# Kernel optimization log

Measured on AMD Instinct MI355X. Metric: run time of the kernel, lower is better.

## Reference

```python
import jax, jax.numpy as jnp
import numpy as np

N_NODES = 50000
N_EDGES = 1600000
HID = 128
NF = 128
NG = 50
NL = 6
CUTOFF = 20.0
NSEG = 64


def _ssp(x):
    # ShiftedSoftplus: softplus(x) - log(2)
    return jax.nn.softplus(x) - jnp.log(2.0).astype(x.dtype)


def setup_inputs() -> dict:
    key = jax.random.key(0)
    ks = jax.random.split(key, 24)
    s = 0.05
    inp = {
        "h": jax.random.normal(ks[0], (N_NODES, HID), dtype=jnp.float32),
        "pos": jax.random.normal(ks[1], (N_NODES, 3), dtype=jnp.float32),
        "edge_index": jax.random.randint(ks[2], (2, N_EDGES), 0, N_NODES, dtype=jnp.int64),
        "batch": jnp.sort(jax.random.randint(ks[3], (N_NODES,), 0, NSEG, dtype=jnp.int64)),
        # per-interaction-block params, stacked over NL layers (weights in [in, out] layout)
        "mlp_w1": jax.random.normal(ks[4], (NL, NG, NF), dtype=jnp.float32) * s,
        "mlp_b1": jnp.zeros((NL, NF), dtype=jnp.float32),
        "mlp_w2": jax.random.normal(ks[5], (NL, NF, NF), dtype=jnp.float32) * s,
        "mlp_b2": jnp.zeros((NL, NF), dtype=jnp.float32),
        "conv_lin1_w": jax.random.normal(ks[6], (NL, HID, NF), dtype=jnp.float32) * s,  # no bias
        "conv_lin2_w": jax.random.normal(ks[7], (NL, NF, HID), dtype=jnp.float32) * s,
        "conv_lin2_b": jnp.zeros((NL, HID), dtype=jnp.float32),
        "lin_w": jax.random.normal(ks[8], (NL, HID, HID), dtype=jnp.float32) * s,
        "lin_b": jnp.zeros((NL, HID), dtype=jnp.float32),
        # readout head
        "out1_w": jax.random.normal(ks[9], (HID, HID // 2), dtype=jnp.float32) * s,
        "out1_b": jnp.zeros((HID // 2,), dtype=jnp.float32),
        "out2_w": jax.random.normal(ks[10], (HID // 2, 1), dtype=jnp.float32) * s,
        "out2_b": jnp.zeros((1,), dtype=jnp.float32),
    }
    return inp


def reference(h, pos, edge_index, batch, mlp_w1, mlp_b1, mlp_w2, mlp_b2,
              conv_lin1_w, conv_lin2_w, conv_lin2_b, lin_w, lin_b,
              out1_w, out1_b, out2_w, out2_b):
    src = edge_index[0]  # j (messages gathered here)
    dst = edge_index[1]  # i (messages aggregated here)
    n = h.shape[0]

    # edge distances from positions (RadiusInteractionGraph.forward)
    diff = pos[src] - pos[dst]                       # [E, 3]
    d = jnp.sqrt(jnp.sum(diff * diff, axis=-1))      # [E]

    # GaussianSmearing
    offset = jnp.linspace(0.0, CUTOFF, NG, dtype=h.dtype)
    coeff = -0.5 / (offset[1] - offset[0]) ** 2
    edge_attr = jnp.exp(coeff * (d[:, None] - offset[None, :]) ** 2)  # [E, NG]

    # cosine cutoff envelope
    C = 0.5 * (jnp.cos(d * jnp.pi / CUTOFF) + 1.0)   # [E]

    for l in range(NL):
        # continuous filter from edge features
        W = _ssp(edge_attr @ mlp_w1[l] + mlp_b1[l]) @ mlp_w2[l] + mlp_b2[l]  # [E, NF]
        W = W * C[:, None]
        # CFConv: lin1 -> gather x_j -> * W -> scatter-add -> lin2
        hx = h @ conv_lin1_w[l]                       # [N, NF]
        msg = hx[src] * W                             # [E, NF]
        agg = jax.ops.segment_sum(msg, dst, num_segments=n)  # [N, NF]
        hc = agg @ conv_lin2_w[l] + conv_lin2_b[l]    # [N, HID]
        # InteractionBlock: act then lin, residual add in SchNet.forward
        h = h + (_ssp(hc) @ lin_w[l] + lin_b[l])

    # readout head
    o = _ssp(h @ out1_w + out1_b) @ out2_w + out2_b   # [N, 1]
    # 'add' readout over molecules
    return jax.ops.segment_sum(o, batch, num_segments=NSEG)  # [NSEG, 1]
```

## Files before the change

### kernel.cpp

```cpp
#include <hip/hip_runtime.h>
#include <math.h>

#define N_NODES 50000
#define N_EDGES 1600000
#define HID 128
#define NF 128
#define NG 50
#define NL 6
#define NSEG 64
#define TAB2 4096
#define CUTOFF 20.0f
#define LOG2F_ 0.6931471805599453f

typedef unsigned short u16;
typedef __attribute__((ext_vector_type(8))) short short8;
typedef __attribute__((ext_vector_type(8))) unsigned short ushort8;
typedef __attribute__((ext_vector_type(4))) float f32x4;

__device__ __forceinline__ float ssp(float x){
  float sp = fmaxf(x, 0.f) + log1pf(expf(-fabsf(x)));
  return sp - LOG2F_;
}
__device__ __forceinline__ float b2f(u16 u){
  unsigned v = ((unsigned)u) << 16; float f; __builtin_memcpy(&f, &v, 4); return f;
}
__device__ __forceinline__ u16 f2b(float f){
  unsigned u; __builtin_memcpy(&u, &f, 4);
  u += 0x7FFFu + ((u >> 16) & 1u);
  return (u16)(u >> 16);
}
__device__ __forceinline__ int swz(int row, int colb){
  return row*256 + (colb ^ ((row & 15) << 4));
}

__global__ __launch_bounds__(256) void k_dist(const int* __restrict__ ei,
                                              const float* __restrict__ pos,
                                              float* __restrict__ dist,
                                              int* __restrict__ deg){
  for (int e = blockIdx.x*blockDim.x + threadIdx.x; e < N_EDGES; e += gridDim.x*blockDim.x){
    int s = ei[e], t = ei[N_EDGES + e];
    float dx = pos[3*s]   - pos[3*t];
    float dy = pos[3*s+1] - pos[3*t+1];
    float dz = pos[3*s+2] - pos[3*t+2];
    dist[e] = sqrtf(dx*dx + dy*dy + dz*dz);
    atomicAdd(&deg[t], 1);
  }
}

__global__ __launch_bounds__(1024) void k_scan(const int* __restrict__ deg, int* __restrict__ row_start){
  __shared__ int sums[1024];
  const int t = threadIdx.x;
  const int CH = (N_NODES + 1023) / 1024;
  const int base = t * CH;
  int s = 0;
  for (int i = 0; i < CH; i++){ int idx = base + i; if (idx < N_NODES) s += deg[idx]; }
  sums[t] = s; __syncthreads();
  for (int off = 1; off < 1024; off <<= 1){
    int v = (t >= off) ? sums[t - off] : 0;
    __syncthreads();
    sums[t] += v;
    __syncthreads();
  }
  int run = (t == 0) ? 0 : sums[t - 1];
  for (int i = 0; i < CH; i++){
    int idx = base + i;
    if (idx < N_NODES){ row_start[idx] = run; run += deg[idx]; }
  }
  if (t == 1023) row_start[N_NODES] = run;
}

__global__ __launch_bounds__(256) void k_scatter(const int* __restrict__ ei,
                                                 const float* __restrict__ dist,
                                                 const int* __restrict__ row_start,
                                                 int* __restrict__ cursor,
                                                 unsigned* __restrict__ csr_pack){
  const float INV_STEP = (TAB2 - 1) / CUTOFF;
  for (int e = blockIdx.x*blockDim.x + threadIdx.x; e < N_EDGES; e += gridDim.x*blockDim.x){
    int dn = ei[N_EDGES + e];
    int slot = atomicAdd(&cursor[dn], 1);
    int p = row_start[dn] + slot;
    int j = (int)(dist[e] * INV_STEP + 0.5f);
    if (j > TAB2 - 1) j = TAB2 - 1;
    csr_pack[p] = ((unsigned)j << 16) | (unsigned)ei[e];
  }
}

__global__ __launch_bounds__(128) void k_table(const float* __restrict__ w1, const float* __restrict__ b1,
                                               const float* __restrict__ w2, const float* __restrict__ b2,
                                               u16* __restrict__ tab){
  int l = blockIdx.x / TAB2, j = blockIdx.x % TAB2;
  int tid = threadIdx.x;
  float d = j * (CUTOFF / (TAB2 - 1));
  __shared__ float ea[NG];
  __shared__ float sbuf[NF];
  if (tid < NG){
    const float gstep = CUTOFF / (NG - 1);
    const float coeff = -0.5f / (gstep * gstep);
    float u = d - tid * gstep;
    ea[tid] = expf(coeff * u * u);
  }
  __syncthreads();
  float z = b1[l*NF + tid];
  for (int k = 0; k < NG; k++) z += ea[k] * w1[(l*NG + k)*NF + tid];
  sbuf[tid] = ssp(z);
  __syncthreads();
  float W = b2[l*NF + tid];
  for (int k = 0; k < NF; k++) W += sbuf[k] * w2[(l*NF + k)*NF + tid];
  float C = 0.5f * (cosf(d * (float)M_PI / CUTOFF) + 1.f);
  tab[((size_t)l*TAB2 + j)*NF + tid] = f2b(W * C);
}

__global__ __launch_bounds__(128) void k_wconv(const float* __restrict__ w, u16* __restrict__ wT){
  int m = blockIdx.x >> 7, o = blockIdx.x & 127;
  int i = threadIdx.x;
  wT[((size_t)m*128 + o)*128 + i] = f2b(w[((size_t)m*128 + i)*128 + o]);
}
__global__ __launch_bounds__(128) void k_wconv64(const float* __restrict__ w, u16* __restrict__ wT){
  int o = blockIdx.x;
  int i = threadIdx.x;
  wT[o*128 + i] = f2b(w[i*64 + o]);
}

__global__ __launch_bounds__(256) void k_lin1m(const float* __restrict__ h,
                                               const u16* __restrict__ w1T,
                                               u16* __restrict__ hxb){
  int tid = threadIdx.x;
  int wv = tid >> 6, l = tid & 63;
  int n0 = blockIdx.x * 64 + wv * 16;
  if (n0 >= N_NODES) return;
  int li = l & 15, lh = l >> 4;
  __shared__ u16 tiles[4][16*128];
  char* tb = (char*)&tiles[wv][0];

  short8 a[4];
  #pragma unroll
  for (int kc = 0; kc < 4; kc++){
    const float* p = &h[(size_t)(n0 + li)*HID + kc*32 + lh*8];
    union { short8 v; u16 u[8]; } t;
    #pragma unroll
    for (int e = 0; e < 8; e++) t.u[e] = f2b(p[e]);
    a[kc] = t.v;
  }
  #pragma unroll
  for (int fc = 0; fc < 8; fc++){
    f32x4 acc = {0.f,0.f,0.f,0.f};
    #pragma unroll
    for (int kc = 0; kc < 4; kc++){
      short8 b = *(const short8*)&w1T[(size_t)(fc*16 + li)*HID + kc*32 + lh*8];
      acc = __builtin_amdgcn_mfma_f32_16x16x32_bf16(a[kc], b, acc, 0, 0, 0);
    }
    #pragma unroll
    for (int r = 0; r < 4; r++)
      *(u16*)(tb + swz(lh*4 + r, fc*32 + li*2)) = f2b(acc[r]);
  }
  #pragma unroll
  for (int g = 0; g < 4; g++){
    int row = g*4 + lh;
    short8 v = *(const short8*)(tb + swz(row, li*16));
    *(short8*)&hxb[(size_t)(n0 + row)*NF + li*8] = v;
  }
}

__global__ __launch_bounds__(256) void k_edgeagg(const int* __restrict__ row_start,
                                                 const unsigned* __restrict__ csr_pack,
                                                 const u16* __restrict__ tab_l,
                                                 const u16* __restrict__ hxb,
                                                 u16* __restrict__ aggb){
  int wave = threadIdx.x >> 6, lane = threadIdx.x & 63;
  int i = blockIdx.x * 4 + wave;
  int li = lane & 15, g = lane >> 4;
  int rs = row_start[i], re = row_start[i + 1];
  float acc0[8], acc1[8];
  #pragma unroll
  for (int r = 0; r < 8; r++){ acc0[r] = 0.f; acc1[r] = 0.f; }
  for (int p = rs + g; p < re; p += 8){
    int p1 = p + 4;
    bool ok1 = p1 < re;
    unsigned v0 = csr_pack[p];
    unsigned v1 = ok1 ? csr_pack[p1] : 0u;
    int s0 = (int)(v0 & 0xFFFFu), j0 = (int)(v0 >> 16);
    ushort8 hv0 = *(const ushort8*)&hxb[(size_t)s0 * NF + li*8];
    ushort8 wv0 = *(const ushort8*)&tab_l[(size_t)j0 * NF + li*8];
    if (ok1){
      int s1 = (int)(v1 & 0xFFFFu), j1 = (int)(v1 >> 16);
      ushort8 hv1 = *(const ushort8*)&hxb[(size_t)s1 * NF + li*8];
      ushort8 wv1 = *(const ushort8*)&tab_l[(size_t)j1 * NF + li*8];
      #pragma unroll
      for (int r = 0; r < 8; r++)
        acc1[r] += b2f(hv1[r]) * b2f(wv1[r]);
    }
    #pragma unroll
    for (int r = 0; r < 8; r++)
      acc0[r] += b2f(hv0[r]) * b2f(wv0[r]);
  }
  #pragma unroll
  for (int r = 0; r < 8; r++){
    float a = acc0[r] + acc1[r];
    a += __shfl_xor(a, 16);
    a += __shfl_xor(a, 32);
    acc0[r] = a;
  }
  if (g == 0){
    union { short8 v; u16 u[8]; } o;
    #pragma unroll
    for (int r = 0; r < 8; r++) o.u[r] = f2b(acc0[r]);
    *(short8*)&aggb[(size_t)i * NF + li*8] = o.v;
  }
}

__global__ __launch_bounds__(256) void k_nodefuse(const u16* __restrict__ aggb,
                                                  const u16* __restrict__ w2T, const float* __restrict__ b2b,
                                                  const u16* __restrict__ lT,  const float* __restrict__ linb,
                                                  float* __restrict__ h,
                                                  const u16* __restrict__ w1nT,
                                                  u16* __restrict__ hxb){
  int tid = threadIdx.x;
  int wv = tid >> 6, l = tid & 63;
  int n0 = blockIdx.x * 64 + wv * 16;
  if (n0 >= N_NODES) return;
  int li = l & 15, lh = l >> 4;
  __shared__ u16 tiles[4][16*128];
  char* tb = (char*)&tiles[wv][0];

  short8 a[4];
  #pragma unroll
  for (int kc = 0; kc < 4; kc++)
    a[kc] = *(const short8*)&aggb[(size_t)(n0 + li)*NF + kc*32 + lh*8];

  #pragma unroll
  for (int fc = 0; fc < 8; fc++){
    f32x4 acc = {0.f,0.f,0.f,0.f};
    #pragma unroll
    for (int kc = 0; kc < 4; kc++){
      short8 b = *(const short8*)&w2T[(size_t)(fc*16 + li)*NF + kc*32 + lh*8];
      acc = __builtin_amdgcn_mfma_f32_16x16x32_bf16(a[kc], b, acc, 0, 0, 0);
    }
    float bias = b2b[fc*16 + li];
    #pragma unroll
    for (int r = 0; r < 4; r++){
      float s = ssp(acc[r] + bias);
      *(u16*)(tb + swz(lh*4 + r, fc*32 + li*2)) = f2b(s);
    }
  }

  short8 a2[4];
  #pragma unroll
  for (int kc = 0; kc < 4; kc++)
    a2[kc] = *(const short8*)(tb + swz(li, kc*64 + lh*16));

  #pragma unroll
  for (int fc = 0; fc < 8; fc++){
    f32x4 acc = {0.f,0.f,0.f,0.f};
    #pragma unroll
    for (int kc = 0; kc < 4; kc++){
      short8 b = *(const short8*)&lT[(size_t)(fc*16 + li)*HID + kc*32 + lh*8];
      acc = __builtin_amdgcn_mfma_f32_16x16x32_bf16(a2[kc], b, acc, 0, 0, 0);
    }
    float bias = linb[fc*16 + li];
    #pragma unroll
    for (int r = 0; r < 4; r++){
      int i = lh*4 + r;
      size_t off = (size_t)(n0 + i)*HID + fc*16 + li;
      float hn = h[off] + acc[r] + bias;
      h[off] = hn;
      if (w1nT) *(u16*)(tb + swz(i, fc*32 + li*2)) = f2b(hn);
    }
  }
  if (!w1nT) return;

  short8 a3[4];
  #pragma unroll
  for (int kc = 0; kc < 4; kc++)
    a3[kc] = *(const short8*)(tb + swz(li, kc*64 + lh*16));
  #pragma unroll
  for (int fc = 0; fc < 8; fc++){
    f32x4 acc = {0.f,0.f,0.f,0.f};
    #pragma unroll
    for (int kc = 0; kc < 4; kc++){
      short8 b = *(const short8*)&w1nT[(size_t)(fc*16 + li)*HID + kc*32 + lh*8];
      acc = __builtin_amdgcn_mfma_f32_16x16x32_bf16(a3[kc], b, acc, 0, 0, 0);
    }
    #pragma unroll
    for (int r = 0; r < 4; r++)
      *(u16*)(tb + swz(lh*4 + r, fc*32 + li*2)) = f2b(acc[r]);
  }
  #pragma unroll
  for (int g = 0; g < 4; g++){
    int row = g*4 + lh;
    short8 v = *(const short8*)(tb + swz(row, li*16));
    *(short8*)&hxb[(size_t)(n0 + row)*NF + li*8] = v;
  }
}

__global__ __launch_bounds__(256) void k_out(const float* __restrict__ h,
                                             const u16* __restrict__ o1wT, const float* __restrict__ b1,
                                             const float* __restrict__ w2, const float* __restrict__ b2,
                                             const int* __restrict__ batch, float* __restrict__ out){
  int tid = threadIdx.x;
  int wv = tid >> 6, l = tid & 63;
  int base = blockIdx.x * 64 + wv * 16;
  if (base >= N_NODES) return;
  int li = l & 15, lh = l >> 4;
  __shared__ float o_s[4][16];

  short8 a[4];
  #pragma unroll
  for (int kc = 0; kc < 4; kc++){
    const float* p = &h[(size_t)(base + li)*HID + kc*32 + lh*8];
    union { short8 v; u16 u[8]; } t;
    #pragma unroll
    for (int e = 0; e < 8; e++) t.u[e] = f2b(p[e]);
    a[kc] = t.v;
  }
  float psum[4] = {0.f,0.f,0.f,0.f};
  #pragma unroll
  for (int fc = 0; fc < 4; fc++){
    f32x4 acc = {0.f,0.f,0.f,0.f};
    #pragma unroll
    for (int kc = 0; kc < 4; kc++){
      short8 b = *(const short8*)&o1wT[(size_t)(fc*16 + li)*HID + kc*32 + lh*8];
      acc = __builtin_amdgcn_mfma_f32_16x16x32_bf16(a[kc], b, acc, 0, 0, 0);
    }
    int col = fc*16 + li;
    float bias = b1[col], w2v = w2[col];
    #pragma unroll
    for (int r = 0; r < 4; r++)
      psum[r] += ssp(acc[r] + bias) * w2v;
  }
  #pragma unroll
  for (int r = 0; r < 4; r++){
    psum[r] += __shfl_xor(psum[r], 1);
    psum[r] += __shfl_xor(psum[r], 2);
    psum[r] += __shfl_xor(psum[r], 4);
    psum[r] += __shfl_xor(psum[r], 8);
  }
  float b2v = b2[0];
  if (li == 0){
    #pragma unroll
    for (int r = 0; r < 4; r++) o_s[wv][lh*4 + r] = psum[r] + b2v;
  }
  float v = o_s[wv][li];
  int n2 = base + li;
  int seg = batch[n2];
  int segn = (li < 15) ? batch[n2 + 1] : -1;
  #pragma unroll
  for (int off = 1; off <= 8; off <<= 1){
    float vv = __shfl_up(v, off);
    int   ss = __shfl_up(seg, off);
    if (li >= off && ss == seg) v += vv;
  }
  if (l < 16 && (li == 15 || segn != seg)) atomicAdd(&out[seg], v);
}

extern "C" void kernel_launch(void* const* d_in, const int* in_sizes, int n_in,
                              void* d_out, int out_size, void* d_ws, size_t ws_size,
                              hipStream_t stream) {
  const float* h     = (const float*)d_in[0];
  const float* pos   = (const float*)d_in[1];
  const int*   ei    = (const int*)d_in[2];
  const int*   batch = (const int*)d_in[3];
  const float* mlp_w1 = (const float*)d_in[4];
  const float* mlp_b1 = (const float*)d_in[5];
  const float* mlp_w2 = (const float*)d_in[6];
  const float* mlp_b2 = (const float*)d_in[7];
  const float* cl1w  = (const float*)d_in[8];
  const float* cl2w  = (const float*)d_in[9];
  const float* cl2b  = (const float*)d_in[10];
  const float* linw  = (const float*)d_in[11];
  const float* linb  = (const float*)d_in[12];
  const float* o1w   = (const float*)d_in[13];
  const float* o1b   = (const float*)d_in[14];
  const float* o2w   = (const float*)d_in[15];
  const float* o2b   = (const float*)d_in[16];
  float* out = (float*)d_out;

  char* ws = (char*)d_ws;
  size_t off = 0;
  float* h_cur = (float*)(ws + off); off += (size_t)N_NODES*HID*4;
  float* dist  = (float*)(ws + off); off += (size_t)N_EDGES*4;
  u16*   aggb  = (u16*)  (ws + off); off += (size_t)N_NODES*NF*2;
  u16*   hxb   = (u16*)  (ws + off); off += (size_t)N_NODES*NF*2;
  u16*   tab   = (u16*)  (ws + off); off += (size_t)NL*TAB2*NF*2;
  u16*   w1T   = (u16*)  (ws + off); off += (size_t)NL*HID*NF*2;
  u16*   w2T   = (u16*)  (ws + off); off += (size_t)NL*NF*HID*2;
  u16*   lT    = (u16*)  (ws + off); off += (size_t)NL*HID*HID*2;
  u16*   o1wT  = (u16*)  (ws + off); off += (size_t)64*HID*2;
  unsigned* csr_pack = (unsigned*)(ws + off); off += (size_t)N_EDGES*4;
  int* deg       = (int*)(ws + off); off += (size_t)N_NODES*4;
  int* row_start = (int*)(ws + off); off += (size_t)(N_NODES + 64)*4;
  int* cursor    = (int*)(ws + off); off += (size_t)N_NODES*4;

  hipMemsetAsync(out, 0, NSEG*sizeof(float), stream);
  hipMemsetAsync(deg, 0, N_NODES*sizeof(int), stream);
  hipMemsetAsync(cursor, 0, N_NODES*sizeof(int), stream);
  hipMemcpyAsync(h_cur, h, (size_t)N_NODES*HID*sizeof(float), hipMemcpyDeviceToDevice, stream);

  k_dist<<<2048, 256, 0, stream>>>(ei, pos, dist, deg);
  k_scan<<<1, 1024, 0, stream>>>(deg, row_start);
  k_scatter<<<2048, 256, 0, stream>>>(ei, dist, row_start, cursor, csr_pack);
  k_table<<<NL*TAB2, 128, 0, stream>>>(mlp_w1, mlp_b1, mlp_w2, mlp_b2, tab);
  k_wconv<<<NL*128, 128, 0, stream>>>(cl1w, w1T);
  k_wconv<<<NL*128, 128, 0, stream>>>(cl2w, w2T);
  k_wconv<<<NL*128, 128, 0, stream>>>(linw, lT);
  k_wconv64<<<64, 128, 0, stream>>>(o1w, o1wT);

  const int NBLK = (N_NODES + 63) / 64;
  k_lin1m<<<NBLK, 256, 0, stream>>>(h_cur, w1T, hxb);
  for (int l = 0; l < NL; l++){
    k_edgeagg<<<N_NODES/4, 256, 0, stream>>>(row_start, csr_pack,
                                             tab + (size_t)l*TAB2*NF, hxb, aggb);
    const u16* w1n = (l + 1 < NL) ? (w1T + (size_t)(l+1)*HID*NF) : nullptr;
    k_nodefuse<<<NBLK, 256, 0, stream>>>(aggb, w2T + (size_t)l*NF*HID, cl2b + (size_t)l*HID,
                                         lT + (size_t)l*HID*HID, linb + (size_t)l*HID,
                                         h_cur, w1n, hxb);
  }
  k_out<<<NBLK, 256, 0, stream>>>(h_cur, o1wT, o1b, o2w, o2b, batch, out);
}
```

Measured before the change: 1.039 ms.

## Restructure CSR build: vectorized histogram, multi-block scan, fuse distance into scatter

Splits the old distance+degree kernel so the degree histogram reads only destination indices with int4 loads, replaces the single-block serial scan with a two-level multi-block warp-shuffle scan, and computes distances inside the scatter kernel, which removes the intermediate dist buffer. The scatter writes packed CSR entries with nontemporal stores. This removes one round trip of per-edge distances through memory and the single-block scan bottleneck, at the cost of an extra kernel launch and recomputing positions in scatter.

```diff
diff --git a/kernel.cpp b/kernel.cpp
--- a/kernel.cpp
+++ b/kernel.cpp
@@ -33,55 +33,82 @@
   return row*256 + (colb ^ ((row & 15) << 4));
 }
 
-__global__ __launch_bounds__(256) void k_dist(const int* __restrict__ ei,
-                                              const float* __restrict__ pos,
-                                              float* __restrict__ dist,
+__global__ __launch_bounds__(256) void k_hist(const int* __restrict__ ei_dst,
                                               int* __restrict__ deg){
+  int e4 = blockIdx.x*blockDim.x + threadIdx.x;
+  if (e4 < N_EDGES/4){
+    int4 d = ((const int4*)ei_dst)[e4];
+    atomicAdd(&deg[d.x], 1);
+    atomicAdd(&deg[d.y], 1);
+    atomicAdd(&deg[d.z], 1);
+    atomicAdd(&deg[d.w], 1);
+  }
+}
+
+__global__ __launch_bounds__(1024) void k_scan1(const int* __restrict__ deg,
+                                                int* __restrict__ row_start,
+                                                int* __restrict__ bsum){
+  int i = blockIdx.x*1024 + threadIdx.x;
+  int lane = threadIdx.x & 63, w = threadIdx.x >> 6;
+  int x = (i < N_NODES) ? deg[i] : 0;
+  int v = x;
+  #pragma unroll
+  for (int off = 1; off < 64; off <<= 1){
+    int t = __shfl_up(v, off);
+    if (lane >= off) v += t;
+  }
+  __shared__ int ws[16];
+  if (lane == 63) ws[w] = v;
+  __syncthreads();
+  if (w == 0 && lane < 16){
+    int t = ws[lane];
+    #pragma unroll
+    for (int off = 1; off < 16; off <<= 1){
+      int u = __shfl_up(t, off);
+      if (lane >= off) t += u;
+    }
+    ws[lane] = t;
+  }
+  __syncthreads();
+  int woff = (w > 0) ? ws[w-1] : 0;
+  if (i < N_NODES) row_start[i] = woff + v - x;
+  if (threadIdx.x == 1023) bsum[blockIdx.x] = woff + v;
+}
+
+__global__ __launch_bounds__(1024) void k_scan2(const int* __restrict__ bsum,
+                                                int* __restrict__ row_start){
+  __shared__ int boff_s;
+  if (threadIdx.x < 64){
+    int lane = threadIdx.x;
+    int acc = 0;
+    for (int b = lane; b < blockIdx.x; b += 64) acc += bsum[b];
+    #pragma unroll
+    for (int off = 32; off >= 1; off >>= 1) acc += __shfl_xor(acc, off);
+    if (lane == 0) boff_s = acc;
+  }
+  __syncthreads();
+  int i = blockIdx.x*1024 + threadIdx.x;
+  if (i < N_NODES) row_start[i] += boff_s;
+  if (i == 0) row_start[N_NODES] = N_EDGES;
+}
+
+__global__ __launch_bounds__(256) void k_scatter(const int* __restrict__ ei,
+                                                 const float* __restrict__ pos,
+                                                 const int* __restrict__ row_start,
+                                                 int* __restrict__ cursor,
+                                                 unsigned* __restrict__ csr_pack){
+  const float INV_STEP = (TAB2 - 1) / CUTOFF;
   for (int e = blockIdx.x*blockDim.x + threadIdx.x; e < N_EDGES; e += gridDim.x*blockDim.x){
     int s = ei[e], t = ei[N_EDGES + e];
     float dx = pos[3*s]   - pos[3*t];
     float dy = pos[3*s+1] - pos[3*t+1];
     float dz = pos[3*s+2] - pos[3*t+2];
-    dist[e] = sqrtf(dx*dx + dy*dy + dz*dz);
-    atomicAdd(&deg[t], 1);
-  }
-}
-
-__global__ __launch_bounds__(1024) void k_scan(const int* __restrict__ deg, int* __restrict__ row_start){
-  __shared__ int sums[1024];
-  const int t = threadIdx.x;
-  const int CH = (N_NODES + 1023) / 1024;
-  const int base = t * CH;
-  int s = 0;
-  for (int i = 0; i < CH; i++){ int idx = base + i; if (idx < N_NODES) s += deg[idx]; }
-  sums[t] = s; __syncthreads();
-  for (int off = 1; off < 1024; off <<= 1){
-    int v = (t >= off) ? sums[t - off] : 0;
-    __syncthreads();
-    sums[t] += v;
-    __syncthreads();
-  }
-  int run = (t == 0) ? 0 : sums[t - 1];
-  for (int i = 0; i < CH; i++){
-    int idx = base + i;
-    if (idx < N_NODES){ row_start[idx] = run; run += deg[idx]; }
-  }
-  if (t == 1023) row_start[N_NODES] = run;
-}
-
-__global__ __launch_bounds__(256) void k_scatter(const int* __restrict__ ei,
-                                                 const float* __restrict__ dist,
-                                                 const int* __restrict__ row_start,
-                                                 int* __restrict__ cursor,
-                                                 unsigned* __restrict__ csr_pack){
-  const float INV_STEP = (TAB2 - 1) / CUTOFF;
-  for (int e = blockIdx.x*blockDim.x + threadIdx.x; e < N_EDGES; e += gridDim.x*blockDim.x){
-    int dn = ei[N_EDGES + e];
-    int slot = atomicAdd(&cursor[dn], 1);
-    int p = row_start[dn] + slot;
-    int j = (int)(dist[e] * INV_STEP + 0.5f);
+    float d = sqrtf(dx*dx + dy*dy + dz*dz);
+    int j = (int)(d * INV_STEP + 0.5f);
     if (j > TAB2 - 1) j = TAB2 - 1;
-    csr_pack[p] = ((unsigned)j << 16) | (unsigned)ei[e];
+    int slot = atomicAdd(&cursor[t], 1);
+    int p = row_start[t] + slot;
+    __builtin_nontemporal_store(((unsigned)j << 16) | (unsigned)s, &csr_pack[p]);
   }
 }
 
@@ -377,7 +404,6 @@
   char* ws = (char*)d_ws;
   size_t off = 0;
   float* h_cur = (float*)(ws + off); off += (size_t)N_NODES*HID*4;
-  float* dist  = (float*)(ws + off); off += (size_t)N_EDGES*4;
   u16*   aggb  = (u16*)  (ws + off); off += (size_t)N_NODES*NF*2;
   u16*   hxb   = (u16*)  (ws + off); off += (size_t)N_NODES*NF*2;
   u16*   tab   = (u16*)  (ws + off); off += (size_t)NL*TAB2*NF*2;
@@ -385,19 +411,22 @@
   u16*   w2T   = (u16*)  (ws + off); off += (size_t)NL*NF*HID*2;
   u16*   lT    = (u16*)  (ws + off); off += (size_t)NL*HID*HID*2;
   u16*   o1wT  = (u16*)  (ws + off); off += (size_t)64*HID*2;
-  unsigned* csr_pack = (unsigned*)(ws + off); off += (size_t)N_EDGES*4;
+  unsigned* csr_pack = (unsigned*)(ws + off); off += (size_t)(N_EDGES + 16)*4;
   int* deg       = (int*)(ws + off); off += (size_t)N_NODES*4;
   int* row_start = (int*)(ws + off); off += (size_t)(N_NODES + 64)*4;
   int* cursor    = (int*)(ws + off); off += (size_t)N_NODES*4;
+  int* bsum      = (int*)(ws + off); off += (size_t)64*4;
 
   hipMemsetAsync(out, 0, NSEG*sizeof(float), stream);
   hipMemsetAsync(deg, 0, N_NODES*sizeof(int), stream);
   hipMemsetAsync(cursor, 0, N_NODES*sizeof(int), stream);
   hipMemcpyAsync(h_cur, h, (size_t)N_NODES*HID*sizeof(float), hipMemcpyDeviceToDevice, stream);
 
-  k_dist<<<2048, 256, 0, stream>>>(ei, pos, dist, deg);
-  k_scan<<<1, 1024, 0, stream>>>(deg, row_start);
-  k_scatter<<<2048, 256, 0, stream>>>(ei, dist, row_start, cursor, csr_pack);
+  const int NSB = (N_NODES + 1023) / 1024;
+  k_hist<<<(N_EDGES/4 + 255)/256, 256, 0, stream>>>(ei + N_EDGES, deg);
+  k_scan1<<<NSB, 1024, 0, stream>>>(deg, row_start, bsum);
+  k_scan2<<<NSB, 1024, 0, stream>>>(bsum, row_start);
+  k_scatter<<<2048, 256, 0, stream>>>(ei, pos, row_start, cursor, csr_pack);
   k_table<<<NL*TAB2, 128, 0, stream>>>(mlp_w1, mlp_b1, mlp_w2, mlp_b2, tab);
   k_wconv<<<NL*128, 128, 0, stream>>>(cl1w, w1T);
   k_wconv<<<NL*128, 128, 0, stream>>>(cl2w, w2T);
```

Result: faster. 937.0 us (-9.8%).
